# Optimization experiments

Hardware: AMD Instinct MI355X
Metric: run time of the kernel (lower is better)

## Reference

```python
import jax, jax.numpy as jnp
import numpy as np

B, V, S = 64, 8, 32        # batch, n_views, volume scale
N = 2 * S                  # graph nodes: 2 stacked views x 32 slices
F = S * S                  # node features: flattened 32x32 slice
EPS = 1e-5                 # BatchNorm eps
NEG = -9e15                # SemGraphConv mask value


def setup_inputs() -> dict:
    key = jax.random.key(0)
    ks = jax.random.split(key, 32)
    x = jax.random.normal(ks[0], (B, V, S, S, S), dtype=jnp.float32)
    # derangement over views (original rejects any idx with a fixed point)
    idx = jnp.roll(jnp.arange(V, dtype=jnp.int32), 1)

    def adj_mask(k):
        m = jax.random.bernoulli(k, 0.15, (N, N))
        return (m | jnp.eye(N, dtype=bool)).astype(jnp.int32)

    d = {"x": x, "idx": idx, "adj1": adj_mask(ks[1]), "adj2": adj_mask(ks[2])}
    for c, k0 in zip((1, 2, 3), (3, 10, 17)):
        d[f"W{c}"] = (jax.random.normal(ks[k0], (2, F, F)) * 0.02).astype(jnp.float32)
        d[f"e{c}"] = (jax.random.normal(ks[k0 + 1], (N, N)) * 0.1).astype(jnp.float32)
        d[f"b{c}"] = jnp.zeros((F,), jnp.float32)
        d[f"gamma{c}"] = jnp.ones((F,), jnp.float32)
        d[f"beta{c}"] = jnp.zeros((F,), jnp.float32)
        d[f"rmean{c}"] = jnp.zeros((F,), jnp.float32)
        d[f"rvar{c}"] = jnp.ones((F,), jnp.float32)
    return d


def _sem_gconv(x, W, e, bias, mask):
    # x: [Bv, N, F]; W: [2, F, F]; e, mask: [N, N]
    h0 = jnp.einsum('bnf,fg->bng', x, W[0])
    h1 = jnp.einsum('bnf,fg->bng', x, W[1])
    logits = jnp.where(mask > 0, e, NEG)
    A = jax.nn.softmax(logits, axis=1)
    diag = jnp.diagonal(A)                      # A * I @ h0 == diag(A) * h0
    A_off = A * (1.0 - jnp.eye(N, dtype=A.dtype))
    out = diag[None, :, None] * h0 + jnp.einsum('nm,bmg->bng', A_off, h1)
    return out + bias


def _gblock(x, W, e, b, gamma, beta, rmean, rvar, mask):
    h = _sem_gconv(x, W, e, b, mask)
    # BatchNorm1d over the feature/channel dim (inference form), then ReLU
    h = (h - rmean) * (gamma * jax.lax.rsqrt(rvar + EPS)) + beta
    return jax.nn.relu(h)


def _channel(x, idx, perm_in, perm_out, params, mask):
    xp = jnp.transpose(x, perm_in)                      # [B,V,S,S,S]
    pairs = jnp.stack([xp, xp[:, idx]], axis=2)         # [B,V,2,S,S,S]
    nodes = pairs.reshape(B * V, N, F)                  # [B*V, 64, 1024]
    h = _gblock(nodes, *params, mask)
    h = h.reshape(B, V, 2, S, S, S).mean(axis=2)        # mean over the pair
    return jnp.transpose(h, perm_out)


def reference(x, idx, adj1, adj2,
              W1, e1, b1, gamma1, beta1, rmean1, rvar1,
              W2, e2, b2, gamma2, beta2, rmean2, rvar2,
              W3, e3, b3, gamma3, beta3, rmean3, rvar3):
    p1 = (W1, e1, b1, gamma1, beta1, rmean1, rvar1)
    p2 = (W2, e2, b2, gamma2, beta2, rmean2, rvar2)
    p3 = (W3, e3, b3, gamma3, beta3, rmean3, rvar3)
    c1 = _channel(x, idx, (0, 1, 4, 2, 3), (0, 1, 3, 4, 2), p1, adj1)
    c2 = _channel(x, idx, (0, 1, 2, 3, 4), (0, 1, 2, 3, 4), p2, adj2)
    c3 = _channel(x, idx, (0, 1, 3, 2, 4), (0, 1, 3, 2, 4), p3, adj2)
    return 0.5 * c1 + 0.25 * c2 + 0.25 * c3
```

## Files before the change

### kernel.cpp

```cpp
#include <hip/hip_runtime.h>
#include <stdint.h>

typedef __attribute__((ext_vector_type(8))) short short8;
typedef __attribute__((ext_vector_type(16))) float f32x16;
typedef __attribute__((ext_vector_type(4))) unsigned short ushort4v;

union S8 { short8 v; unsigned short u[8]; };

static __device__ __forceinline__ unsigned short f2bf(float f) {
  union { float f; unsigned u; } v; v.f = f;
  unsigned r = v.u + 0x7fffu + ((v.u >> 16) & 1u);
  return (unsigned short)(r >> 16);
}
static __device__ __forceinline__ float bf2f(unsigned short u) {
  union { unsigned u; float f; } v; v.u = ((unsigned)u) << 16;
  return v.f;
}

static __device__ __forceinline__ void glds16(const void* g, void* l) {
  __builtin_amdgcn_global_load_lds(
      (const __attribute__((address_space(1))) unsigned int*)g,
      (__attribute__((address_space(3))) unsigned int*)l, 16, 0, 0);
}

__global__ __launch_bounds__(256) void prep_w(const float* __restrict__ Wa,
                                              const float* __restrict__ Wb,
                                              const float* __restrict__ Wc,
                                              unsigned short* __restrict__ wfrag) {
  int t    = blockIdx.x * 256 + threadIdx.x;
  int lane = t & 63;
  int tt   = (t >> 6) & 7;
  int ks   = (t >> 9) & 1;
  int kt   = (t >> 10) & 31;
  int g8   = (t >> 15) & 7;
  int c    = t >> 18;
  const float* W = (c == 0) ? Wa : (c == 1) ? Wb : Wc;
  int s  = tt >> 2, gt = tt & 3;
  int g  = g8*128 + gt*32 + (lane & 31);
  int k0 = kt*32 + ks*16 + ((lane >> 5) * 8);
  const float* src = W + (size_t)s * 1048576 + (size_t)k0 * 1024 + g;
  unsigned short* dst = wfrag + (size_t)t * 8;
#pragma unroll
  for (int e = 0; e < 8; ++e) dst[e] = f2bf(src[(size_t)e * 1024]);
}

__global__ __launch_bounds__(256) void prep_x2(const float* __restrict__ x,
                                               int c, unsigned short* __restrict__ ximg) {
  int t = blockIdx.x * 256 + threadIdx.x;
  int lane = t & 63;
  int ks = (t >> 6) & 1;
  int kt = (t >> 7) & 31;
  int vid = t >> 12;
  const float* src = x + (size_t)vid * 32768;
  int i = lane & 31;
  int k0 = kt*32 + ks*16 + ((lane >> 5) * 8);
  S8 pk;
  if (c == 0) {
#pragma unroll
    for (int e = 0; e < 8; ++e) pk.u[e] = f2bf(src[(size_t)(k0 + e)*32 + i]);
  } else {
    const float* sp = (c == 1) ? (src + i*1024 + k0)
                               : (src + (k0 >> 5)*1024 + i*32 + (k0 & 31));
    float4 u0 = *(const float4*)sp, u1 = *(const float4*)(sp + 4);
    pk.u[0]=f2bf(u0.x); pk.u[1]=f2bf(u0.y); pk.u[2]=f2bf(u0.z); pk.u[3]=f2bf(u0.w);
    pk.u[4]=f2bf(u1.x); pk.u[5]=f2bf(u1.y); pk.u[6]=f2bf(u1.z); pk.u[7]=f2bf(u1.w);
  }
  *(short8*)(ximg + (size_t)t * 8) = pk.v;
}

__global__ __launch_bounds__(256) void prep_misc(
    const float* e0, const int* a0, const float* b0, const float* g0, const float* be0, const float* rm0, const float* rv0,
    const float* e1, const int* a1, const float* b1, const float* g1, const float* be1, const float* rm1, const float* rv1,
    const float* e2, const int* a2, const float* b2, const float* g2, const float* be2, const float* rm2, const float* rv2,
    unsigned short* __restrict__ aofrag, float* __restrict__ diagA,
    float* __restrict__ scale2, float* __restrict__ shift2) {
  __shared__ float A[64][64];
  int c = blockIdx.x;
  int tid = threadIdx.x;
  const float* ev = (c==0)?e0:(c==1)?e1:e2;
  const int*   ad = (c==0)?a0:(c==1)?a1:a2;
  const float* bb = (c==0)?b0:(c==1)?b1:b2;
  const float* gm = (c==0)?g0:(c==1)?g1:g2;
  const float* bt = (c==0)?be0:(c==1)?be1:be2;
  const float* rm = (c==0)?rm0:(c==1)?rm1:rm2;
  const float* rv = (c==0)?rv0:(c==1)?rv1:rv2;
  if (tid < 64) {
    int n = tid;
    float mx = -3.0e38f;
    for (int m = 0; m < 64; ++m) {
      float lg = (ad[n*64+m] > 0) ? ev[n*64+m] : -9.0e15f;
      A[n][m] = lg; mx = fmaxf(mx, lg);
    }
    float ssum = 0.f;
    for (int m = 0; m < 64; ++m) { float p = __expf(A[n][m] - mx); A[n][m] = p; ssum += p; }
    float inv = 1.f / ssum;
    for (int m = 0; m < 64; ++m) A[n][m] *= inv;
  }
  __syncthreads();
  if (tid < 64) diagA[c*64 + tid] = A[tid][tid];
  for (int idx = tid; idx < 4096; idx += 256) {
    int e  = idx & 7;
    int l  = (idx >> 3) & 63;
    int ks = (idx >> 9) & 3;
    int nt = idx >> 11;
    int n = nt*32 + (l & 31);
    int m = ks*16 + ((l >> 5) * 8) + e;
    float vv = (m == n) ? 0.f : A[n][m];
    aofrag[c*4096 + idx] = f2bf(vv);
  }
  for (int g = tid; g < 1024; g += 256) {
    float sc = gm[g] * rsqrtf(rv[g] + 1e-5f);
    scale2[c*1024 + g] = sc;
    shift2[c*1024 + g] = bt[g] + (bb[g] - rm[g]) * sc;
  }
}

template<int CH>
__device__ __forceinline__ void loadAfb(float av[2][8], const float* __restrict__ sview,
                                        int d0, int lh, int kt) {
#pragma unroll
  for (int ks = 0; ks < 2; ++ks) {
    int kb = kt*32 + ks*16 + lh*8;
    if (CH == 0) {
#pragma unroll
      for (int e = 0; e < 8; ++e) av[ks][e] = sview[(size_t)(kb + e)*32 + d0];
    } else if (CH == 1) {
      const float* sp = sview + d0*1024 + kb;
      *(float4*)&av[ks][0] = *(const float4*)sp;
      *(float4*)&av[ks][4] = *(const float4*)(sp + 4);
    } else {
      const float* sp = sview + kt*1024 + d0*32 + ks*16 + lh*8;
      *(float4*)&av[ks][0] = *(const float4*)sp;
      *(float4*)&av[ks][4] = *(const float4*)(sp + 4);
    }
  }
}

template<int CH, int IMG>
__global__ __launch_bounds__(512, 1) void gconv(
    const float* __restrict__ x, const int* __restrict__ idxp,
    const unsigned short* __restrict__ wimg, const unsigned short* __restrict__ ximg,
    const unsigned short* __restrict__ aofrag,
    const float* __restrict__ diagA, const float* __restrict__ scale2,
    const float* __restrict__ shift2, float* __restrict__ out) {
  __shared__ alignas(128) char lds[131072];
  int tid = threadIdx.x, lane = tid & 63, wave = tid >> 6;
  int l31 = lane & 31, lh = lane >> 5;
  int wr = wave >> 2, wc = wave & 3;
  int sB = wc >> 1, gp = wc & 1;
  int bid = blockIdx.x;
  int g8 = bid & 7, b = bid >> 3;
  const float* xvw = x + ((size_t)b*8 + wave) * 32768;

  const char* srcA = (const char*)ximg + ((size_t)b*8 + wave)*65536 + lane*16;
  const char* srcB = (const char*)wimg + (size_t)g8*524288 + wave*2048 + lane*16;

  f32x16 acc[4][2];
#pragma unroll
  for (int mt = 0; mt < 4; ++mt)
#pragma unroll
    for (int g2 = 0; g2 < 2; ++g2)
#pragma unroll
      for (int r = 0; r < 16; ++r) acc[mt][g2][r] = 0.f;

  char* p0 = lds; char* p1 = lds + 32768; char* p2 = lds + 65536;
  int tt0 = sB*4 + gp*2;

  auto stageA = [&](char* dst, int t) {
    if (IMG) {
      const char* s = srcA + (size_t)t * 2048;
      glds16(s,        dst + wave*2048);
      glds16(s + 1024, dst + wave*2048 + 1024);
    } else {
      alignas(16) float av[2][8];
      loadAfb<CH>(av, xvw, l31, lh, t);
#pragma unroll
      for (int ks = 0; ks < 2; ++ks) {
        S8 pk;
#pragma unroll
        for (int e = 0; e < 8; ++e) pk.u[e] = f2bf(av[ks][e]);
        *(short8*)(dst + wave*2048 + ks*1024 + lane*16) = pk.v;
      }
    }
  };
  auto stageB = [&](char* dst, int t) {
    const char* s = srcB + (size_t)t * 16384;
    glds16(s,        dst + 16384 + wave*2048);
    glds16(s + 1024, dst + 16384 + wave*2048 + 1024);
  };

#pragma unroll 1
  for (int pre = 0; pre < 1; ++pre) {
    stageA(p0, 0); stageB(p0, 0);
    stageA(p1, 1); stageB(p1, 1);
  }
  if (IMG) asm volatile("s_waitcnt vmcnt(4)" ::: "memory");
  else     asm volatile("s_waitcnt vmcnt(0) lgkmcnt(0)" ::: "memory");
  __builtin_amdgcn_sched_barrier(0);
  __builtin_amdgcn_s_barrier();

#pragma unroll 1
  for (int t = 0; t < 32; ++t) {
    short8 af[4], bfr[2];
#pragma unroll
    for (int mt = 0; mt < 4; ++mt)
      af[mt] = *(const short8*)(p0 + (4*wr + mt)*2048 + lane*16);
#pragma unroll
    for (int g2 = 0; g2 < 2; ++g2)
      bfr[g2] = *(const short8*)(p0 + 16384 + (tt0 + g2)*1024 + lane*16);
    if (t < 30) stageA(p2, t + 2);
    __builtin_amdgcn_s_barrier();
    __builtin_amdgcn_s_setprio(1);
#pragma unroll
    for (int mt = 0; mt < 4; ++mt)
#pragma unroll
      for (int g2 = 0; g2 < 2; ++g2)
        acc[mt][g2] = __builtin_amdgcn_mfma_f32_32x32x16_bf16(af[mt], bfr[g2], acc[mt][g2], 0, 0, 0);
    __builtin_amdgcn_s_setprio(0);
    __builtin_amdgcn_s_barrier();
#pragma unroll
    for (int mt = 0; mt < 4; ++mt)
      af[mt] = *(const short8*)(p0 + (4*wr + mt)*2048 + 1024 + lane*16);
#pragma unroll
    for (int g2 = 0; g2 < 2; ++g2)
      bfr[g2] = *(const short8*)(p0 + 16384 + 8192 + (tt0 + g2)*1024 + lane*16);
    if (t < 30) stageB(p2, t + 2);
    __builtin_amdgcn_s_barrier();
    __builtin_amdgcn_s_setprio(1);
#pragma unroll
    for (int mt = 0; mt < 4; ++mt)
#pragma unroll
      for (int g2 = 0; g2 < 2; ++g2)
        acc[mt][g2] = __builtin_amdgcn_mfma_f32_32x32x16_bf16(af[mt], bfr[g2], acc[mt][g2], 0, 0, 0);
    __builtin_amdgcn_s_setprio(0);
    if (IMG) {
      if (t < 30) asm volatile("s_waitcnt vmcnt(4)" ::: "memory");
      else        asm volatile("s_waitcnt vmcnt(0)" ::: "memory");
    } else {
      asm volatile("s_waitcnt vmcnt(0) lgkmcnt(0)" ::: "memory");
    }
    __builtin_amdgcn_sched_barrier(0);
    __builtin_amdgcn_s_barrier();
    { char* tmp = p0; p0 = p1; p1 = p2; p2 = tmp; }
  }
  __syncthreads();

  char* H1r = lds;
  char* H0r = lds + 65536;
  if (sB == 1) {
#pragma unroll
    for (int mt = 0; mt < 4; ++mt) {
      int vloc = 4*wr + mt;
#pragma unroll
      for (int g2 = 0; g2 < 2; ++g2) {
        int col = gp*64 + g2*32 + l31;
        int xw = (col & 3) << 4;
        char* cb = H1r + vloc*8192 + col*64;
#pragma unroll
        for (int j = 0; j < 4; ++j) {
          ushort4v pk;
          pk.x = f2bf(acc[mt][g2][4*j+0]);
          pk.y = f2bf(acc[mt][g2][4*j+1]);
          pk.z = f2bf(acc[mt][g2][4*j+2]);
          pk.w = f2bf(acc[mt][g2][4*j+3]);
          *(ushort4v*)(cb + ((j*16 + lh*8) ^ xw)) = pk;
        }
      }
    }
  } else {
#pragma unroll
    for (int mt = 0; mt < 4; ++mt) {
      int vloc = 4*wr + mt;
#pragma unroll
      for (int g2 = 0; g2 < 2; ++g2) {
        int gt = gp*2 + g2;
        char* cb = H0r + vloc*8192 + gt*2048 + lane*16;
        S8 lo, hi;
#pragma unroll
        for (int e = 0; e < 8; ++e) { lo.u[e] = f2bf(acc[mt][g2][e]); hi.u[e] = f2bf(acc[mt][g2][8+e]); }
        *(short8*)cb = lo.v;
        *(short8*)(cb + 1024) = hi.v;
      }
    }
  }
  __syncthreads();

  {
    int v = wave;
    int v2 = idxp[v];
    f32x16 agg[2][4];
#pragma unroll
    for (int nt = 0; nt < 2; ++nt)
#pragma unroll
      for (int gt = 0; gt < 4; ++gt)
#pragma unroll
        for (int r = 0; r < 16; ++r) agg[nt][gt][r] = 0.f;

#pragma unroll
    for (int ks = 0; ks < 4; ++ks) {
      int vsel = (ks < 2) ? v : v2;
      int ksl = ks & 1;
      short8 aof0 = *(const short8*)((const char*)aofrag + (size_t)((0*4 + ks)*64 + lane)*16);
      short8 aof1 = *(const short8*)((const char*)aofrag + (size_t)((1*4 + ks)*64 + lane)*16);
#pragma unroll
      for (int gt = 0; gt < 4; ++gt) {
        int col = gt*32 + l31;
        int xw = (col & 3) << 4;
        short8 hf = *(const short8*)(H1r + vsel*8192 + col*64 + ((ksl*32 + lh*16) ^ xw));
        agg[0][gt] = __builtin_amdgcn_mfma_f32_32x32x16_bf16(aof0, hf, agg[0][gt], 0, 0, 0);
        agg[1][gt] = __builtin_amdgcn_mfma_f32_32x32x16_bf16(aof1, hf, agg[1][gt], 0, 0, 0);
      }
    }

    size_t gid = (size_t)b*8 + v;
    size_t obase = gid * 32768;
#pragma unroll
    for (int gt = 0; gt < 4; ++gt) {
      int g = g8*128 + gt*32 + l31;
      float sc = scale2[g], sh = shift2[g];
      S8 h0a0, h0a1, h0b0, h0b1;
      h0a0.v = *(const short8*)(H0r + v *8192 + gt*2048 + lane*16);
      h0a1.v = *(const short8*)(H0r + v *8192 + gt*2048 + 1024 + lane*16);
      h0b0.v = *(const short8*)(H0r + v2*8192 + gt*2048 + lane*16);
      h0b1.v = *(const short8*)(H0r + v2*8192 + gt*2048 + 1024 + lane*16);
#pragma unroll
      for (int j = 0; j < 4; ++j) {
        int i00 = j*8 + lh*4;
        float res[4];
#pragma unroll
        for (int jj = 0; jj < 4; ++jj) {
          int q = j*4 + jj;
          int i = i00 + jj;
          float h0v  = (q < 8) ? bf2f(h0a0.u[q]) : bf2f(h0a1.u[q-8]);
          float h0v2 = (q < 8) ? bf2f(h0b0.u[q]) : bf2f(h0b1.u[q-8]);
          float va = diagA[i]      * h0v  + agg[0][gt][q];
          float vb = diagA[32 + i] * h0v2 + agg[1][gt][q];
          va = fmaxf(va * sc + sh, 0.f);
          vb = fmaxf(vb * sc + sh, 0.f);
          res[jj] = 0.5f * (va + vb);
        }
        if (CH == 0) {
          float4 o4;
          o4.x = 0.5f*res[0]; o4.y = 0.5f*res[1]; o4.z = 0.5f*res[2]; o4.w = 0.5f*res[3];
          *(float4*)(out + obase + (size_t)g*32 + i00) = o4;
        } else if (CH == 1) {
#pragma unroll
          for (int jj = 0; jj < 4; ++jj)
            out[obase + (size_t)(i00 + jj)*1024 + g] += 0.25f * res[jj];
        } else {
#pragma unroll
          for (int jj = 0; jj < 4; ++jj)
            out[obase + (size_t)(g >> 5)*1024 + (size_t)(i00 + jj)*32 + (g & 31)] += 0.25f * res[jj];
        }
      }
    }
  }
}

extern "C" void kernel_launch(void* const* d_in, const int* in_sizes, int n_in,
                              void* d_out, int out_size, void* d_ws, size_t ws_size,
                              hipStream_t stream) {
  (void)in_sizes; (void)n_in; (void)out_size;
  const float* x    = (const float*)d_in[0];
  const int*   idx  = (const int*)d_in[1];
  const int*   adj1 = (const int*)d_in[2];
  const int*   adj2 = (const int*)d_in[3];
  const float *W[3], *e[3], *bb[3], *gm[3], *bt[3], *rm[3], *rv[3];
  for (int c = 0; c < 3; ++c) {
    int base = 4 + c*7;
    W[c]  = (const float*)d_in[base + 0];
    e[c]  = (const float*)d_in[base + 1];
    bb[c] = (const float*)d_in[base + 2];
    gm[c] = (const float*)d_in[base + 3];
    bt[c] = (const float*)d_in[base + 4];
    rm[c] = (const float*)d_in[base + 5];
    rv[c] = (const float*)d_in[base + 6];
  }
  char* ws = (char*)d_ws;
  unsigned short* wfrag  = (unsigned short*)ws;
  unsigned short* aofrag = (unsigned short*)(ws + 12582912);
  float* diagA  = (float*)(ws + 12607488);
  float* scale2 = (float*)(ws + 12608256);
  float* shift2 = (float*)(ws + 12620544);
  unsigned short* ximg = (unsigned short*)(ws + 16777216);
  bool img = ws_size >= (size_t)(16777216 + 33554432);

  prep_w<<<3072, 256, 0, stream>>>(W[0], W[1], W[2], wfrag);
  prep_misc<<<3, 256, 0, stream>>>(
      e[0], adj1, bb[0], gm[0], bt[0], rm[0], rv[0],
      e[1], adj2, bb[1], gm[1], bt[1], rm[1], rv[1],
      e[2], adj2, bb[2], gm[2], bt[2], rm[2], rv[2],
      aofrag, diagA, scale2, shift2);

  float* out = (float*)d_out;
  if (img) {
    prep_x2<<<8192, 256, 0, stream>>>(x, 0, ximg);
    gconv<0,1><<<512, 512, 0, stream>>>(x, idx, wfrag, ximg, aofrag,
                                        diagA, scale2, shift2, out);
    prep_x2<<<8192, 256, 0, stream>>>(x, 1, ximg);
    gconv<1,1><<<512, 512, 0, stream>>>(x, idx, wfrag + 2097152, ximg, aofrag + 4096,
                                        diagA + 64,  scale2 + 1024, shift2 + 1024, out);
    prep_x2<<<8192, 256, 0, stream>>>(x, 2, ximg);
    gconv<2,1><<<512, 512, 0, stream>>>(x, idx, wfrag + 4194304, ximg, aofrag + 8192,
                                        diagA + 128, scale2 + 2048, shift2 + 2048, out);
  } else {
    gconv<0,0><<<512, 512, 0, stream>>>(x, idx, wfrag, ximg, aofrag,
                                        diagA, scale2, shift2, out);
    gconv<1,0><<<512, 512, 0, stream>>>(x, idx, wfrag + 2097152, ximg, aofrag + 4096,
                                        diagA + 64,  scale2 + 1024, shift2 + 1024, out);
    gconv<2,0><<<512, 512, 0, stream>>>(x, idx, wfrag + 4194304, ximg, aofrag + 8192,
                                        diagA + 128, scale2 + 2048, shift2 + 2048, out);
  }
}
```

Baseline: 362.6 us.

## Split gconv blocks in half along output columns for two blocks per CU

Each gconv block now covers 64 output feature columns instead of 128, using 256 threads and 72 KB of LDS. This allows two blocks per CU, and the grid doubles to 1024 blocks. Each wave now stages two views' A tiles, and the aggregation epilogue loops over two views per wave. The aim is better latency hiding and overlap between co-resident blocks. In exchange, the A (activation) tiles are loaded twice as often across the grid, and per-block B traffic is narrower.

```diff
diff --git a/kernel.cpp b/kernel.cpp
--- a/kernel.cpp
+++ b/kernel.cpp
@@ -137,23 +137,23 @@
 }
 
 template<int CH, int IMG>
-__global__ __launch_bounds__(512, 1) void gconv(
+__global__ __launch_bounds__(256, 2) void gconv(
     const float* __restrict__ x, const int* __restrict__ idxp,
     const unsigned short* __restrict__ wimg, const unsigned short* __restrict__ ximg,
     const unsigned short* __restrict__ aofrag,
     const float* __restrict__ diagA, const float* __restrict__ scale2,
     const float* __restrict__ shift2, float* __restrict__ out) {
-  __shared__ alignas(128) char lds[131072];
+  __shared__ alignas(128) char lds[73728];
   int tid = threadIdx.x, lane = tid & 63, wave = tid >> 6;
   int l31 = lane & 31, lh = lane >> 5;
-  int wr = wave >> 2, wc = wave & 3;
-  int sB = wc >> 1, gp = wc & 1;
+  int wr = wave >> 1, sB = wave & 1;
   int bid = blockIdx.x;
-  int g8 = bid & 7, b = bid >> 3;
-  const float* xvw = x + ((size_t)b*8 + wave) * 32768;
-
-  const char* srcA = (const char*)ximg + ((size_t)b*8 + wave)*65536 + lane*16;
-  const char* srcB = (const char*)wimg + (size_t)g8*524288 + wave*2048 + lane*16;
+  int g8 = bid & 7, gp = (bid >> 3) & 1, b = bid >> 4;
+
+  const char* wimgG8 = (const char*)wimg + (size_t)g8 * 524288 + lane*16;
+  const char* srcAw  = (const char*)ximg + ((size_t)b*8 + 2*wave) * 65536 + lane*16;
+  const float* xw0 = x + ((size_t)b*8 + 2*wave) * 32768;
+  const float* xw1 = xw0 + 32768;
 
   f32x16 acc[4][2];
 #pragma unroll
@@ -163,51 +163,54 @@
 #pragma unroll
       for (int r = 0; r < 16; ++r) acc[mt][g2][r] = 0.f;
 
-  char* p0 = lds; char* p1 = lds + 32768; char* p2 = lds + 65536;
-  int tt0 = sB*4 + gp*2;
+  char* p0 = lds; char* p1 = lds + 24576; char* p2 = lds + 49152;
 
   auto stageA = [&](char* dst, int t) {
     if (IMG) {
-      const char* s = srcA + (size_t)t * 2048;
-      glds16(s,        dst + wave*2048);
-      glds16(s + 1024, dst + wave*2048 + 1024);
+#pragma unroll
+      for (int j = 0; j < 4; ++j) {
+        const char* s = srcAw + (size_t)(j >> 1)*65536 + (size_t)t*2048 + (j & 1)*1024;
+        glds16(s, dst + (2*wave + (j >> 1))*2048 + (j & 1)*1024);
+      }
     } else {
-      alignas(16) float av[2][8];
-      loadAfb<CH>(av, xvw, l31, lh, t);
-#pragma unroll
-      for (int ks = 0; ks < 2; ++ks) {
-        S8 pk;
-#pragma unroll
-        for (int e = 0; e < 8; ++e) pk.u[e] = f2bf(av[ks][e]);
-        *(short8*)(dst + wave*2048 + ks*1024 + lane*16) = pk.v;
+#pragma unroll
+      for (int j = 0; j < 2; ++j) {
+        alignas(16) float av[2][8];
+        loadAfb<CH>(av, j ? xw1 : xw0, l31, lh, t);
+#pragma unroll
+        for (int ks = 0; ks < 2; ++ks) {
+          S8 pk;
+#pragma unroll
+          for (int e = 0; e < 8; ++e) pk.u[e] = f2bf(av[ks][e]);
+          *(short8*)(dst + (2*wave + j)*2048 + ks*1024 + lane*16) = pk.v;
+        }
       }
     }
   };
   auto stageB = [&](char* dst, int t) {
-    const char* s = srcB + (size_t)t * 16384;
-    glds16(s,        dst + 16384 + wave*2048);
-    glds16(s + 1024, dst + 16384 + wave*2048 + 1024);
+#pragma unroll
+    for (int jj = 0; jj < 2; ++jj) {
+      const char* s = wimgG8 + (size_t)(((t*2 + (wave >> 1))*8) + (wave & 1)*4 + gp*2 + jj)*1024;
+      glds16(s, dst + 16384 + (wave*2 + jj)*1024);
+    }
   };
 
-#pragma unroll 1
-  for (int pre = 0; pre < 1; ++pre) {
-    stageA(p0, 0); stageB(p0, 0);
-    stageA(p1, 1); stageB(p1, 1);
-  }
-  if (IMG) asm volatile("s_waitcnt vmcnt(4)" ::: "memory");
+  stageA(p0, 0); stageB(p0, 0);
+  stageA(p1, 1); stageB(p1, 1);
+  if (IMG) asm volatile("s_waitcnt vmcnt(6)" ::: "memory");
   else     asm volatile("s_waitcnt vmcnt(0) lgkmcnt(0)" ::: "memory");
   __builtin_amdgcn_sched_barrier(0);
   __builtin_amdgcn_s_barrier();
 
 #pragma unroll 1
   for (int t = 0; t < 32; ++t) {
-    short8 af[4], bfr[2];
+    short8 af[4], bf[2];
 #pragma unroll
     for (int mt = 0; mt < 4; ++mt)
       af[mt] = *(const short8*)(p0 + (4*wr + mt)*2048 + lane*16);
 #pragma unroll
     for (int g2 = 0; g2 < 2; ++g2)
-      bfr[g2] = *(const short8*)(p0 + 16384 + (tt0 + g2)*1024 + lane*16);
+      bf[g2] = *(const short8*)(p0 + 16384 + (sB*2 + g2)*1024 + lane*16);
     if (t < 30) stageA(p2, t + 2);
     __builtin_amdgcn_s_barrier();
     __builtin_amdgcn_s_setprio(1);
@@ -215,7 +218,7 @@
     for (int mt = 0; mt < 4; ++mt)
 #pragma unroll
       for (int g2 = 0; g2 < 2; ++g2)
-        acc[mt][g2] = __builtin_amdgcn_mfma_f32_32x32x16_bf16(af[mt], bfr[g2], acc[mt][g2], 0, 0, 0);
+        acc[mt][g2] = __builtin_amdgcn_mfma_f32_32x32x16_bf16(af[mt], bf[g2], acc[mt][g2], 0, 0, 0);
     __builtin_amdgcn_s_setprio(0);
     __builtin_amdgcn_s_barrier();
 #pragma unroll
@@ -223,7 +226,7 @@
       af[mt] = *(const short8*)(p0 + (4*wr + mt)*2048 + 1024 + lane*16);
 #pragma unroll
     for (int g2 = 0; g2 < 2; ++g2)
-      bfr[g2] = *(const short8*)(p0 + 16384 + 8192 + (tt0 + g2)*1024 + lane*16);
+      bf[g2] = *(const short8*)(p0 + 16384 + ((2 + sB)*2 + g2)*1024 + lane*16);
     if (t < 30) stageB(p2, t + 2);
     __builtin_amdgcn_s_barrier();
     __builtin_amdgcn_s_setprio(1);
@@ -231,10 +234,10 @@
     for (int mt = 0; mt < 4; ++mt)
 #pragma unroll
       for (int g2 = 0; g2 < 2; ++g2)
-        acc[mt][g2] = __builtin_amdgcn_mfma_f32_32x32x16_bf16(af[mt], bfr[g2], acc[mt][g2], 0, 0, 0);
+        acc[mt][g2] = __builtin_amdgcn_mfma_f32_32x32x16_bf16(af[mt], bf[g2], acc[mt][g2], 0, 0, 0);
     __builtin_amdgcn_s_setprio(0);
     if (IMG) {
-      if (t < 30) asm volatile("s_waitcnt vmcnt(4)" ::: "memory");
+      if (t < 30) asm volatile("s_waitcnt vmcnt(6)" ::: "memory");
       else        asm volatile("s_waitcnt vmcnt(0)" ::: "memory");
     } else {
       asm volatile("s_waitcnt vmcnt(0) lgkmcnt(0)" ::: "memory");
@@ -246,16 +249,16 @@
   __syncthreads();
 
   char* H1r = lds;
-  char* H0r = lds + 65536;
+  char* H0r = lds + 32768;
   if (sB == 1) {
 #pragma unroll
     for (int mt = 0; mt < 4; ++mt) {
-      int vloc = 4*wr + mt;
+      int vid = 4*wr + mt;
 #pragma unroll
       for (int g2 = 0; g2 < 2; ++g2) {
-        int col = gp*64 + g2*32 + l31;
+        int col = g2*32 + l31;
         int xw = (col & 3) << 4;
-        char* cb = H1r + vloc*8192 + col*64;
+        char* cb = H1r + vid*4096 + col*64;
 #pragma unroll
         for (int j = 0; j < 4; ++j) {
           ushort4v pk;
@@ -270,11 +273,10 @@
   } else {
 #pragma unroll
     for (int mt = 0; mt < 4; ++mt) {
-      int vloc = 4*wr + mt;
+      int vid = 4*wr + mt;
 #pragma unroll
       for (int g2 = 0; g2 < 2; ++g2) {
-        int gt = gp*2 + g2;
-        char* cb = H0r + vloc*8192 + gt*2048 + lane*16;
+        char* cb = H0r + (size_t)(vid*2 + g2)*2048 + lane*16;
         S8 lo, hi;
 #pragma unroll
         for (int e = 0; e < 8; ++e) { lo.u[e] = f2bf(acc[mt][g2][e]); hi.u[e] = f2bf(acc[mt][g2][8+e]); }
@@ -285,16 +287,17 @@
   }
   __syncthreads();
 
-  {
-    int v = wave;
+#pragma unroll 1
+  for (int vg = 0; vg < 2; ++vg) {
+    int v = wave*2 + vg;
     int v2 = idxp[v];
-    f32x16 agg[2][4];
+    f32x16 agg[2][2];
 #pragma unroll
     for (int nt = 0; nt < 2; ++nt)
 #pragma unroll
-      for (int gt = 0; gt < 4; ++gt)
-#pragma unroll
-        for (int r = 0; r < 16; ++r) agg[nt][gt][r] = 0.f;
+      for (int g2 = 0; g2 < 2; ++g2)
+#pragma unroll
+        for (int r = 0; r < 16; ++r) agg[nt][g2][r] = 0.f;
 
 #pragma unroll
     for (int ks = 0; ks < 4; ++ks) {
@@ -303,26 +306,26 @@
       short8 aof0 = *(const short8*)((const char*)aofrag + (size_t)((0*4 + ks)*64 + lane)*16);
       short8 aof1 = *(const short8*)((const char*)aofrag + (size_t)((1*4 + ks)*64 + lane)*16);
 #pragma unroll
-      for (int gt = 0; gt < 4; ++gt) {
-        int col = gt*32 + l31;
+      for (int g2 = 0; g2 < 2; ++g2) {
+        int col = g2*32 + l31;
         int xw = (col & 3) << 4;
-        short8 hf = *(const short8*)(H1r + vsel*8192 + col*64 + ((ksl*32 + lh*16) ^ xw));
-        agg[0][gt] = __builtin_amdgcn_mfma_f32_32x32x16_bf16(aof0, hf, agg[0][gt], 0, 0, 0);
-        agg[1][gt] = __builtin_amdgcn_mfma_f32_32x32x16_bf16(aof1, hf, agg[1][gt], 0, 0, 0);
+        short8 hf = *(const short8*)(H1r + vsel*4096 + col*64 + ((ksl*32 + lh*16) ^ xw));
+        agg[0][g2] = __builtin_amdgcn_mfma_f32_32x32x16_bf16(aof0, hf, agg[0][g2], 0, 0, 0);
+        agg[1][g2] = __builtin_amdgcn_mfma_f32_32x32x16_bf16(aof1, hf, agg[1][g2], 0, 0, 0);
       }
     }
 
     size_t gid = (size_t)b*8 + v;
     size_t obase = gid * 32768;
 #pragma unroll
-    for (int gt = 0; gt < 4; ++gt) {
-      int g = g8*128 + gt*32 + l31;
+    for (int g2 = 0; g2 < 2; ++g2) {
+      int g = g8*128 + gp*64 + g2*32 + l31;
       float sc = scale2[g], sh = shift2[g];
       S8 h0a0, h0a1, h0b0, h0b1;
-      h0a0.v = *(const short8*)(H0r + v *8192 + gt*2048 + lane*16);
-      h0a1.v = *(const short8*)(H0r + v *8192 + gt*2048 + 1024 + lane*16);
-      h0b0.v = *(const short8*)(H0r + v2*8192 + gt*2048 + lane*16);
-      h0b1.v = *(const short8*)(H0r + v2*8192 + gt*2048 + 1024 + lane*16);
+      h0a0.v = *(const short8*)(H0r + (size_t)(v *2 + g2)*2048 + lane*16);
+      h0a1.v = *(const short8*)(H0r + (size_t)(v *2 + g2)*2048 + 1024 + lane*16);
+      h0b0.v = *(const short8*)(H0r + (size_t)(v2*2 + g2)*2048 + lane*16);
+      h0b1.v = *(const short8*)(H0r + (size_t)(v2*2 + g2)*2048 + 1024 + lane*16);
 #pragma unroll
       for (int j = 0; j < 4; ++j) {
         int i00 = j*8 + lh*4;
@@ -333,8 +336,8 @@
           int i = i00 + jj;
           float h0v  = (q < 8) ? bf2f(h0a0.u[q]) : bf2f(h0a1.u[q-8]);
           float h0v2 = (q < 8) ? bf2f(h0b0.u[q]) : bf2f(h0b1.u[q-8]);
-          float va = diagA[i]      * h0v  + agg[0][gt][q];
-          float vb = diagA[32 + i] * h0v2 + agg[1][gt][q];
+          float va = diagA[i]      * h0v  + agg[0][g2][q];
+          float vb = diagA[32 + i] * h0v2 + agg[1][g2][q];
           va = fmaxf(va * sc + sh, 0.f);
           vb = fmaxf(vb * sc + sh, 0.f);
           res[jj] = 0.5f * (va + vb);
@@ -395,20 +398,20 @@
   float* out = (float*)d_out;
   if (img) {
     prep_x2<<<8192, 256, 0, stream>>>(x, 0, ximg);
-    gconv<0,1><<<512, 512, 0, stream>>>(x, idx, wfrag, ximg, aofrag,
-                                        diagA, scale2, shift2, out);
+    gconv<0,1><<<1024, 256, 0, stream>>>(x, idx, wfrag, ximg, aofrag,
+                                         diagA, scale2, shift2, out);
     prep_x2<<<8192, 256, 0, stream>>>(x, 1, ximg);
-    gconv<1,1><<<512, 512, 0, stream>>>(x, idx, wfrag + 2097152, ximg, aofrag + 4096,
-                                        diagA + 64,  scale2 + 1024, shift2 + 1024, out);
+    gconv<1,1><<<1024, 256, 0, stream>>>(x, idx, wfrag + 2097152, ximg, aofrag + 4096,
+                                         diagA + 64,  scale2 + 1024, shift2 + 1024, out);
     prep_x2<<<8192, 256, 0, stream>>>(x, 2, ximg);
-    gconv<2,1><<<512, 512, 0, stream>>>(x, idx, wfrag + 4194304, ximg, aofrag + 8192,
-                                        diagA + 128, scale2 + 2048, shift2 + 2048, out);
+    gconv<2,1><<<1024, 256, 0, stream>>>(x, idx, wfrag + 4194304, ximg, aofrag + 8192,
+                                         diagA + 128, scale2 + 2048, shift2 + 2048, out);
   } else {
-    gconv<0,0><<<512, 512, 0, stream>>>(x, idx, wfrag, ximg, aofrag,
-                                        diagA, scale2, shift2, out);
-    gconv<1,0><<<512, 512, 0, stream>>>(x, idx, wfrag + 2097152, ximg, aofrag + 4096,
-                                        diagA + 64,  scale2 + 1024, shift2 + 1024, out);
-    gconv<2,0><<<512, 512, 0, stream>>>(x, idx, wfrag + 4194304, ximg, aofrag + 8192,
-                                        diagA + 128, scale2 + 2048, shift2 + 2048, out);
-  }
-}
+    gconv<0,0><<<1024, 256, 0, stream>>>(x, idx, wfrag, ximg, aofrag,
+                                         diagA, scale2, shift2, out);
+    gconv<1,0><<<1024, 256, 0, stream>>>(x, idx, wfrag + 2097152, ximg, aofrag + 4096,
+                                         diagA + 64,  scale2 + 1024, shift2 + 1024, out);
+    gconv<2,0><<<1024, 256, 0, stream>>>(x, idx, wfrag + 4194304, ximg, aofrag + 8192,
+                                         diagA + 128, scale2 + 2048, shift2 + 2048, out);
+  }
+}
```

Result: faster. 321.9 us (-11.2%).
